# Performance work log

Hardware: AMD Instinct MI355X
Metric: run time of the kernel (lower is better)

The kernel has to match this reference:

```python
import jax, jax.numpy as jnp
import numpy as np

S = 14
C = 20
STEP = 1.0 / 14
LAMBDA_COORD = 3.0
LAMBDA_NOOBJ = 0.3
LAMBDA_OBJ = 1.0
LAMBDA_CLS = 1.5


def setup_inputs() -> dict:
    key = jax.random.key(0)
    k1, k2 = jax.random.split(key)
    batch = 4096
    pred = jax.random.normal(k1, (batch, S, S, 30), dtype=jnp.float32)
    target = jax.random.normal(k2, (batch, S, S, 30), dtype=jnp.float32)
    return {"pred": pred, "target": target}


def _convert_boxes(box):
    # box: [B, S, S, 2, 4] in (cx, cy, w, h) grid-relative coords
    # grid index i is the x (third) axis, j the y (second) axis, per forward's [x, y]
    gi = jnp.arange(S, dtype=box.dtype)[None, None, :, None]  # x index
    gj = jnp.arange(S, dtype=box.dtype)[None, :, None, None]  # y index
    x = (box[..., 0] + gi) * STEP - box[..., 2] * 0.5
    y = (box[..., 1] + gj) * STEP - box[..., 3] * 0.5
    out = jnp.stack([x, y, box[..., 2], box[..., 3]], axis=-1)
    return jnp.maximum(out, 0.0)  # torch.clamp(box, min=0) on the whole box


def _iou(b1, b2):
    x1, y1, w1, h1 = b1[..., 0], b1[..., 1], b1[..., 2], b1[..., 3]
    x2, y2, w2, h2 = b2[..., 0], b2[..., 1], b2[..., 2], b2[..., 3]
    inter_w = jnp.maximum(w1 + w2 - (jnp.maximum(x1 + w1, x2 + w2) - jnp.minimum(x1, x2)), 0.0)
    inter_h = jnp.maximum(h1 + h2 - (jnp.maximum(y1 + h1, y2 + h2) - jnp.minimum(y1, y2)), 0.0)
    inter = inter_w * inter_h
    union = w1 * h1 + w2 * h2 - inter
    return inter / (union + 1e-6)


def _smooth_l1_sum(p, t, mask):
    d = p - t
    ad = jnp.abs(d)
    l = jnp.where(ad < 1.0, 0.5 * d * d, ad - 0.5)
    return jnp.sum(l * mask)


def reference(pred, target):
    batch = pred.shape[0]
    pb = pred[..., :10].reshape(batch, S, S, 2, 5)
    tb = target[..., :10].reshape(batch, S, S, 2, 5)
    pred_cls = pred[..., 10:]
    target_cls = target[..., 10:]

    obj_mask = tb[..., 4] > 0          # [B,S,S,2]
    sig_mask = obj_mask[..., 1]         # [B,S,S]

    # responsible-box selection: elementwise IoU between pred box k and target box k
    ious = _iou(_convert_boxes(pb[..., :4]), _convert_boxes(tb[..., :4]))  # [B,S,S,2]
    max_i = jnp.argmax(ious, axis=-1)   # first-max, matches torch .max(0)
    keep = jnp.arange(2) == max_i[..., None]
    obj_mask = jnp.where(sig_mask[..., None], obj_mask & keep, obj_mask)
    noobj_mask = ~obj_mask

    om = obj_mask.astype(pred.dtype)
    nm = noobj_mask.astype(pred.dtype)

    conf_sq = (pb[..., 4] - tb[..., 4]) ** 2
    noobj_loss = jnp.sum(conf_sq * nm)
    obj_loss = jnp.sum(conf_sq * om)

    xy_loss = _smooth_l1_sum(pb[..., :2], tb[..., :2], om[..., None])
    wh_loss = _smooth_l1_sum(
        jnp.sqrt(jnp.maximum(pb[..., 2:4], 1e-6)),
        jnp.sqrt(jnp.maximum(tb[..., 2:4], 1e-6)),
        om[..., None],
    )

    logp = jax.nn.log_softmax(pred_cls, axis=-1)
    tgt_idx = jnp.argmax(target_cls, axis=-1)  # [B,S,S]
    nll = -jnp.take_along_axis(logp, tgt_idx[..., None], axis=-1)[..., 0]
    class_loss = jnp.sum(nll * sig_mask.astype(pred.dtype))

    total = (LAMBDA_COORD * (xy_loss + wh_loss)
             + LAMBDA_OBJ * obj_loss
             + LAMBDA_NOOBJ * noobj_loss
             + LAMBDA_CLS * class_loss) / batch
    return total
```

## Files before the change

kernel.cpp:

```cpp
#include <hip/hip_runtime.h>
#include <math.h>

#define SS 14
#define NCLS 20
#define CELL_FLOATS 30
#define BLOCK 256
#define CELLS_PER_BLOCK 256
#define FPB (CELLS_PER_BLOCK * CELL_FLOATS)
#define F4PB (FPB / 4)

__device__ __forceinline__ float smooth_l1(float d) {
    float ad = fabsf(d);
    return ad < 1.0f ? 0.5f * d * d : ad - 0.5f;
}

__device__ __forceinline__ void conv_box(const float* b, float gi, float gj,
                                         float& x, float& y, float& w, float& h) {
    const float STEP = 1.0f / 14.0f;
    x = fmaxf((b[0] + gi) * STEP - b[2] * 0.5f, 0.0f);
    y = fmaxf((b[1] + gj) * STEP - b[3] * 0.5f, 0.0f);
    w = fmaxf(b[2], 0.0f);
    h = fmaxf(b[3], 0.0f);
}

__device__ __forceinline__ float iou_box(float x1, float y1, float w1, float h1,
                                         float x2, float y2, float w2, float h2) {
    float iw = fmaxf(w1 + w2 - (fmaxf(x1 + w1, x2 + w2) - fminf(x1, x2)), 0.0f);
    float ih = fmaxf(h1 + h2 - (fmaxf(y1 + h1, y2 + h2) - fminf(y1, y2)), 0.0f);
    float inter = iw * ih;
    float uni = w1 * h1 + w2 * h2 - inter;
    return inter / (uni + 1e-6f);
}

__global__ void zero_out_kernel(float* out) { out[0] = 0.0f; }

__global__ __launch_bounds__(BLOCK) void yolo_loss_kernel(
    const float4* __restrict__ pred4, const float4* __restrict__ target4,
    float* __restrict__ out, int ncells, float inv_batch) {
    __shared__ float sp[FPB];
    __shared__ float st[FPB];

    const int tid = threadIdx.x;
    const int cell0 = blockIdx.x * CELLS_PER_BLOCK;
    const long long total4 = ((long long)ncells * CELL_FLOATS) / 4;
    const long long base4 = (long long)blockIdx.x * F4PB;

#pragma unroll
    for (int k = 0; k < 8; ++k) {
        int i = tid + k * BLOCK;
        if (i < F4PB && base4 + i < total4) {
            ((float4*)sp)[i] = pred4[base4 + i];
            ((float4*)st)[i] = target4[base4 + i];
        }
    }
    __syncthreads();

    int cell = cell0 + tid;
    float tot = 0.0f;
    if (cell < ncells) {
        float p[CELL_FLOATS], t[CELL_FLOATS];
        const float2* pp = (const float2*)(sp + tid * CELL_FLOATS);
        const float2* tp = (const float2*)(st + tid * CELL_FLOATS);
#pragma unroll
        for (int k = 0; k < CELL_FLOATS / 2; ++k) {
            ((float2*)p)[k] = pp[k];
            ((float2*)t)[k] = tp[k];
        }

        int rc = cell % (SS * SS);
        float gj = (float)(rc / SS);
        float gi = (float)(rc % SS);

        float px, py, pw, ph, tx, ty, tw, th;
        conv_box(p + 0, gi, gj, px, py, pw, ph);
        conv_box(t + 0, gi, gj, tx, ty, tw, th);
        float iou0 = iou_box(px, py, pw, ph, tx, ty, tw, th);
        conv_box(p + 5, gi, gj, px, py, pw, ph);
        conv_box(t + 5, gi, gj, tx, ty, tw, th);
        float iou1 = iou_box(px, py, pw, ph, tx, ty, tw, th);

        bool obj0 = t[4] > 0.0f;
        bool obj1 = t[9] > 0.0f;
        bool sig = obj1;
        bool m1 = iou1 > iou0;
        bool om0 = sig ? (obj0 && !m1) : obj0;
        bool om1 = sig ? m1 : false;

        float c0 = p[4] - t[4]; c0 *= c0;
        float c1 = p[9] - t[9]; c1 *= c1;
        float obj_l = (om0 ? c0 : 0.0f) + (om1 ? c1 : 0.0f);
        float noobj_l = (om0 ? 0.0f : c0) + (om1 ? 0.0f : c1);

        float xy = 0.0f, wh = 0.0f;
        if (om0) {
            xy += smooth_l1(p[0] - t[0]) + smooth_l1(p[1] - t[1]);
            wh += smooth_l1(sqrtf(fmaxf(p[2], 1e-6f)) - sqrtf(fmaxf(t[2], 1e-6f)));
            wh += smooth_l1(sqrtf(fmaxf(p[3], 1e-6f)) - sqrtf(fmaxf(t[3], 1e-6f)));
        }
        if (om1) {
            xy += smooth_l1(p[5] - t[5]) + smooth_l1(p[6] - t[6]);
            wh += smooth_l1(sqrtf(fmaxf(p[7], 1e-6f)) - sqrtf(fmaxf(t[7], 1e-6f)));
            wh += smooth_l1(sqrtf(fmaxf(p[8], 1e-6f)) - sqrtf(fmaxf(t[8], 1e-6f)));
        }

        float cls = 0.0f;
        {
            float m = p[10];
#pragma unroll
            for (int c = 1; c < NCLS; ++c) m = fmaxf(m, p[10 + c]);
            float se = 0.0f;
#pragma unroll
            for (int c = 0; c < NCLS; ++c) se += expf(p[10 + c] - m);
            float bt = t[10];
            int bi = 0;
#pragma unroll
            for (int c = 1; c < NCLS; ++c) {
                if (t[10 + c] > bt) { bt = t[10 + c]; bi = c; }
            }
            float logp = p[10 + bi] - m - logf(se);
            cls = sig ? -logp : 0.0f;
        }

        tot = 3.0f * (xy + wh) + obj_l + 0.3f * noobj_l + 1.5f * cls;
        tot *= inv_batch;
    }

#pragma unroll
    for (int off = 32; off > 0; off >>= 1) tot += __shfl_down(tot, off, 64);
    __shared__ float wsum[4];
    int lane = threadIdx.x & 63;
    int wid = threadIdx.x >> 6;
    if (lane == 0) wsum[wid] = tot;
    __syncthreads();
    if (threadIdx.x == 0) {
        float s = wsum[0] + wsum[1] + wsum[2] + wsum[3];
        atomicAdd(out, s);
    }
}

extern "C" void kernel_launch(void* const* d_in, const int* in_sizes, int n_in,
                              void* d_out, int out_size, void* d_ws, size_t ws_size,
                              hipStream_t stream) {
    const float4* pred4 = (const float4*)d_in[0];
    const float4* target4 = (const float4*)d_in[1];
    float* out = (float*)d_out;

    int total = in_sizes[0];
    int ncells = total / CELL_FLOATS;
    int batch = ncells / (SS * SS);
    float inv_batch = 1.0f / (float)batch;

    zero_out_kernel<<<1, 1, 0, stream>>>(out);
    int grid = (ncells + CELLS_PER_BLOCK - 1) / CELLS_PER_BLOCK;
    yolo_loss_kernel<<<grid, BLOCK, 0, stream>>>(pred4, target4, out, ncells, inv_batch);
}
```

Before: 234.2 us.

## Halve cells per block and replace atomic accumulation with two-stage reduction

Each block now stages 128 cells instead of 256, so shared memory per block halves and occupancy should rise, but only half of the 256 threads do the per-cell compute. The single-address atomicAdd is replaced by per-block partial sums in the workspace plus a one-block final reduction kernel, which also removes the zero-init launch. This avoids atomic contention over roughly 6272 blocks. The cost is an extra launch and a serial strided read of the partials by one block.

```diff
diff --git a/kernel.cpp b/kernel.cpp
--- a/kernel.cpp
+++ b/kernel.cpp
@@ -5,8 +5,8 @@
 #define NCLS 20
 #define CELL_FLOATS 30
 #define BLOCK 256
-#define CELLS_PER_BLOCK 256
-#define FPB (CELLS_PER_BLOCK * CELL_FLOATS)
+#define CPB 128
+#define FPB (CPB * CELL_FLOATS)
 #define F4PB (FPB / 4)
 
 __device__ __forceinline__ float smooth_l1(float d) {
@@ -32,21 +32,18 @@
     return inter / (uni + 1e-6f);
 }
 
-__global__ void zero_out_kernel(float* out) { out[0] = 0.0f; }
-
 __global__ __launch_bounds__(BLOCK) void yolo_loss_kernel(
     const float4* __restrict__ pred4, const float4* __restrict__ target4,
-    float* __restrict__ out, int ncells, float inv_batch) {
+    float* __restrict__ partials, int ncells, float inv_batch) {
     __shared__ float sp[FPB];
     __shared__ float st[FPB];
 
     const int tid = threadIdx.x;
-    const int cell0 = blockIdx.x * CELLS_PER_BLOCK;
     const long long total4 = ((long long)ncells * CELL_FLOATS) / 4;
     const long long base4 = (long long)blockIdx.x * F4PB;
 
 #pragma unroll
-    for (int k = 0; k < 8; ++k) {
+    for (int k = 0; k < 4; ++k) {
         int i = tid + k * BLOCK;
         if (i < F4PB && base4 + i < total4) {
             ((float4*)sp)[i] = pred4[base4 + i];
@@ -55,9 +52,9 @@
     }
     __syncthreads();
 
-    int cell = cell0 + tid;
+    int cell = blockIdx.x * CPB + tid;
     float tot = 0.0f;
-    if (cell < ncells) {
+    if (tid < CPB && cell < ncells) {
         float p[CELL_FLOATS], t[CELL_FLOATS];
         const float2* pp = (const float2*)(sp + tid * CELL_FLOATS);
         const float2* tp = (const float2*)(st + tid * CELL_FLOATS);
@@ -133,9 +130,22 @@
     if (lane == 0) wsum[wid] = tot;
     __syncthreads();
     if (threadIdx.x == 0) {
-        float s = wsum[0] + wsum[1] + wsum[2] + wsum[3];
-        atomicAdd(out, s);
+        partials[blockIdx.x] = wsum[0] + wsum[1] + wsum[2] + wsum[3];
     }
+}
+
+__global__ __launch_bounds__(BLOCK) void reduce_kernel(
+    const float* __restrict__ partials, float* __restrict__ out, int n) {
+    float s = 0.0f;
+    for (int i = threadIdx.x; i < n; i += BLOCK) s += partials[i];
+#pragma unroll
+    for (int off = 32; off > 0; off >>= 1) s += __shfl_down(s, off, 64);
+    __shared__ float wsum[4];
+    int lane = threadIdx.x & 63;
+    int wid = threadIdx.x >> 6;
+    if (lane == 0) wsum[wid] = s;
+    __syncthreads();
+    if (threadIdx.x == 0) out[0] = wsum[0] + wsum[1] + wsum[2] + wsum[3];
 }
 
 extern "C" void kernel_launch(void* const* d_in, const int* in_sizes, int n_in,
@@ -144,13 +154,14 @@
     const float4* pred4 = (const float4*)d_in[0];
     const float4* target4 = (const float4*)d_in[1];
     float* out = (float*)d_out;
+    float* partials = (float*)d_ws;
 
     int total = in_sizes[0];
     int ncells = total / CELL_FLOATS;
     int batch = ncells / (SS * SS);
     float inv_batch = 1.0f / (float)batch;
 
-    zero_out_kernel<<<1, 1, 0, stream>>>(out);
-    int grid = (ncells + CELLS_PER_BLOCK - 1) / CELLS_PER_BLOCK;
-    yolo_loss_kernel<<<grid, BLOCK, 0, stream>>>(pred4, target4, out, ncells, inv_batch);
+    int grid = (ncells + CPB - 1) / CPB;
+    yolo_loss_kernel<<<grid, BLOCK, 0, stream>>>(pred4, target4, partials, ncells, inv_batch);
+    reduce_kernel<<<1, BLOCK, 0, stream>>>(partials, out, grid);
 }
```

Result: no change. 230.9 us (-1.4%).
